# Kernel optimization log

Measured on AMD Instinct MI355X. Metric: run time of the kernel, lower is better.

The kernel has to match this reference:

```python
import jax, jax.numpy as jnp
import numpy as np

EPS = 1e-08
SURROGATE_SCALE = 10.0  # SuperSpike surrogate slope

@jax.custom_vjp
def spike_fn(v):
    # Heaviside forward, SuperSpike surrogate gradient backward
    return (v > 0).astype(v.dtype)

def _spike_fwd(v):
    return spike_fn(v), v

def _spike_bwd(v, g):
    return (g / (1.0 + SURROGATE_SCALE * jnp.abs(v)) ** 2,)

spike_fn.defvjp(_spike_fwd, _spike_bwd)


def setup_inputs() -> dict:
    key = jax.random.key(0)
    k1, k2, k3, k4 = jax.random.split(key, 4)
    B, C, T = 64, 256, 2048
    x = jax.random.normal(k1, (B, C, T), dtype=jnp.float32)
    conv_weight = jax.random.normal(k2, (C, C, 3), dtype=jnp.float32) * 0.05
    beta = jnp.clip(0.7 + 0.01 * jax.random.normal(k3, (1,), dtype=jnp.float32), 0.0, 1.0)
    b = jnp.clip(1.0 + 0.01 * jax.random.normal(k4, (C,), dtype=jnp.float32), 0.0, None)
    return {"x": x, "conv_weight": conv_weight, "beta": beta, "b": b}


def reference(x, conv_weight, beta, b):
    # x: (B, C, T); LIF recurrence over T with scaled threshold/reset
    norm = (conv_weight ** 2).sum((1, 2))          # (C,)
    inv_norm = 1.0 / (norm + EPS)                   # (C,)
    B, C, T = x.shape
    xt = jnp.transpose(x, (2, 0, 1))                # (T, B, C)

    def step(carry, inp):
        mem, spk = carry
        rst = spk * (b * norm)                      # einsum ab,b,b->ab
        mem = (mem - rst) * beta + inp * (1.0 - beta)
        mthr = mem * inv_norm - b
        spk = spike_fn(mthr)
        return (mem, spk), spk

    init = (jnp.zeros((B, C), x.dtype), jnp.zeros((B, C), x.dtype))
    _, spk_rec = jax.lax.scan(step, init, xt)       # (T, B, C)
    return jnp.transpose(spk_rec, (1, 2, 0))        # (B, C, T), flatten_output=False
```

## Files before the change

kernel.cpp:

```cpp
#include <hip/hip_runtime.h>

#define C_DIM 256
#define T_DIM 2048
#define B_DIM 64
#define NROWS (B_DIM * C_DIM)
#define SEGS 8
#define SEGL (T_DIM / SEGS)
#define WARM 128
#define PW   32
#define NPH  ((WARM + SEGL) / PW)
#define WARM_PH (WARM / PW)
#define NSTR 64
#define BUF_F (NSTR * PW)

__device__ __forceinline__ float sqrn(float v) { return __fmul_rn(v, v); }

__global__ __launch_bounds__(64) void norm_kernel(const float* __restrict__ w,
                                                  const float* __restrict__ b,
                                                  float* __restrict__ bn,
                                                  float* __restrict__ ninv) {
    const int c = blockIdx.x;
    const int k = threadIdx.x;
    __shared__ float q[8];
    if (k < 8) {
        const float* a = w + c * 768 + k * 96;
        float r0 = sqrn(a[0]), r1 = sqrn(a[1]), r2 = sqrn(a[2]), r3 = sqrn(a[3]);
        float r4 = sqrn(a[4]), r5 = sqrn(a[5]), r6 = sqrn(a[6]), r7 = sqrn(a[7]);
        #pragma unroll
        for (int i = 8; i < 96; i += 8) {
            r0 = __fadd_rn(r0, sqrn(a[i + 0]));
            r1 = __fadd_rn(r1, sqrn(a[i + 1]));
            r2 = __fadd_rn(r2, sqrn(a[i + 2]));
            r3 = __fadd_rn(r3, sqrn(a[i + 3]));
            r4 = __fadd_rn(r4, sqrn(a[i + 4]));
            r5 = __fadd_rn(r5, sqrn(a[i + 5]));
            r6 = __fadd_rn(r6, sqrn(a[i + 6]));
            r7 = __fadd_rn(r7, sqrn(a[i + 7]));
        }
        q[k] = __fadd_rn(__fadd_rn(__fadd_rn(r0, r1), __fadd_rn(r2, r3)),
                         __fadd_rn(__fadd_rn(r4, r5), __fadd_rn(r6, r7)));
    }
    __syncthreads();
    if (k == 0) {
        float s = __fadd_rn(__fadd_rn(__fadd_rn(q[0], q[1]), __fadd_rn(q[2], q[3])),
                            __fadd_rn(__fadd_rn(q[4], q[5]), __fadd_rn(q[6], q[7])));
        bn[c]   = __fmul_rn(b[c], s);
        ninv[c] = 1.0f / __fadd_rn(s, 1e-8f);
    }
}

__device__ __forceinline__ float step_fast(float xw, float& mem, int& mask,
                                           float bnc, float beta, float nic, float bc) {
    float m0 = __fmul_rn(mem, beta);
    float m1 = __fmul_rn(__fsub_rn(mem, bnc), beta);
    m0 = __fadd_rn(m0, xw);
    m1 = __fadd_rn(m1, xw);
    int mi = (__float_as_int(m1) & mask) | (__float_as_int(m0) & ~mask);
    mem = __int_as_float(mi);
    float p = __fmul_rn(mem, nic);
    float d = __fsub_rn(bc, p);
    mask = __float_as_int(d) >> 31;
    return __int_as_float(mask & 0x3f800000);
}

#define STEP4_NOSTORE(v)                                                   \
    do {                                                                   \
        float xw0 = __fmul_rn((v).x, omb);                                 \
        float xw1 = __fmul_rn((v).y, omb);                                 \
        float xw2 = __fmul_rn((v).z, omb);                                 \
        float xw3 = __fmul_rn((v).w, omb);                                 \
        (void)step_fast(xw0, mem, mask, bnc, beta, nic, bc);               \
        (void)step_fast(xw1, mem, mask, bnc, beta, nic, bc);               \
        (void)step_fast(xw2, mem, mask, bnc, beta, nic, bc);               \
        (void)step_fast(xw3, mem, mask, bnc, beta, nic, bc);               \
    } while (0)

#define STEP4_STORE(v, o)                                                  \
    do {                                                                   \
        float xw0 = __fmul_rn((v).x, omb);                                 \
        float xw1 = __fmul_rn((v).y, omb);                                 \
        float xw2 = __fmul_rn((v).z, omb);                                 \
        float xw3 = __fmul_rn((v).w, omb);                                 \
        (o).x = step_fast(xw0, mem, mask, bnc, beta, nic, bc);             \
        (o).y = step_fast(xw1, mem, mask, bnc, beta, nic, bc);             \
        (o).z = step_fast(xw2, mem, mask, bnc, beta, nic, bc);             \
        (o).w = step_fast(xw3, mem, mask, bnc, beta, nic, bc);             \
    } while (0)

#define WAITCNT_LGKM0  0xC07F
#define WAITVM8()  asm volatile("s_waitcnt vmcnt(8)" ::: "memory")
#define WAITVM16() asm volatile("s_waitcnt vmcnt(16)" ::: "memory")

__device__ __forceinline__ void dma16(const float* gp, float* lp) {
    __builtin_amdgcn_global_load_lds(
        (const __attribute__((address_space(1))) void*)gp,
        (__attribute__((address_space(3))) void*)lp,
        16, 0, 0);
}

__global__ __launch_bounds__(64)
void lif_seg_kernel(const float* __restrict__ x,
                    const float* __restrict__ beta_p,
                    const float* __restrict__ b,
                    const float* __restrict__ bn,
                    const float* __restrict__ ninv,
                    float* __restrict__ out) {
    __shared__ __align__(16) float lds[2 * BUF_F];

    const int lane = threadIdx.x;
    const int seg  = lane & 7;
    const int row  = blockIdx.x * 8 + (lane >> 3);
    const int c    = row & (C_DIM - 1);
    const int lk   = lane & 7;

    const int ds  = lane >> 3;
    const int du  = lane & 7;
    const int swz = du ^ ds;

    const float beta = beta_p[0];
    const float omb  = __fsub_rn(1.0f, beta);
    const float bnc  = bn[c];
    const float nic  = ninv[c];
    const float bc   = b[c];

    float mem = 0.0f;
    int   mask = 0;

    {
        int rel = ds * SEGL - WARM;
        if (rel < 0) rel = 0;
        const float* g = x + rel + 4 * swz;
        #pragma unroll
        for (int q = 0; q < 8; ++q) {
            const size_t grow = (size_t)(blockIdx.x * 8 + q);
            dma16(g + grow * T_DIM, lds + q * (8 * PW));
        }
    }

    #pragma unroll 1
    for (int P = 0; P < NPH; ++P) {
        const int cur = P & 1;
        float* buf = lds + cur * BUF_F;

        if (P + 1 < NPH) {
            int rel = ds * SEGL - WARM + (P + 1) * PW;
            if (rel < 0) rel = 0;
            const float* g = x + rel + 4 * swz;
            float* dst = lds + (cur ^ 1) * BUF_F;
            #pragma unroll
            for (int q = 0; q < 8; ++q) {
                const size_t grow = (size_t)(blockIdx.x * 8 + q);
                dma16(g + grow * T_DIM, dst + q * (8 * PW));
            }
        }

        if (P <= WARM_PH || P == NPH - 1) { WAITVM8(); } else { WAITVM16(); }

        float* my = buf + lane * PW;

        if (P < WARM_PH) {
            #pragma unroll
            for (int g = 0; g < PW / 4; ++g) {
                float4 v = *(const float4*)(my + 4 * (g ^ lk));
                STEP4_NOSTORE(v);
            }
            if (P == WARM_PH - 1) {
                if (seg == 0) { mem = 0.0f; mask = 0; }
            }
        } else {
            #pragma unroll
            for (int g = 0; g < PW / 4; ++g) {
                float4 v = *(const float4*)(my + 4 * (g ^ lk));
                float4 o;
                STEP4_STORE(v, o);
                *(float4*)(my + 4 * (g ^ lk)) = o;
            }
            __builtin_amdgcn_s_waitcnt(WAITCNT_LGKM0);

            const int rel = ds * SEGL - WARM + P * PW;
            #pragma unroll
            for (int q = 0; q < 8; ++q) {
                const size_t grow = (size_t)(blockIdx.x * 8 + q);
                float4 v = *(const float4*)(buf + (8 * q + ds) * PW + 4 * swz);
                *(float4*)(out + grow * T_DIM + rel + 4 * du) = v;
            }
        }
    }
}

extern "C" void kernel_launch(void* const* d_in, const int* in_sizes, int n_in,
                              void* d_out, int out_size, void* d_ws, size_t ws_size,
                              hipStream_t stream) {
    const float* x    = (const float*)d_in[0];
    const float* w    = (const float*)d_in[1];
    const float* beta = (const float*)d_in[2];
    const float* b    = (const float*)d_in[3];
    float* out  = (float*)d_out;
    float* bn   = (float*)d_ws;
    float* ninv = bn + C_DIM;

    norm_kernel<<<C_DIM, 64, 0, stream>>>(w, b, bn, ninv);
    lif_seg_kernel<<<(NROWS * SEGS) / NSTR, NSTR, 0, stream>>>(x, beta, b, bn, ninv, out);
}
```

Baseline: 255.3 us.

## Deepen LDS DMA pipeline to four buffers with smaller phase width

Halves the per-phase time window to 16 steps and switches from double buffering to a 4-deep ring of LDS buffers with three phases of global-to-LDS DMA in flight. The load and store mapping changes to a new XOR swizzle, and the vmcnt waits are retuned per phase. The goal is to hide more global memory latency behind the serial recurrence. In exchange there are twice as many phases, each carrying loop, wait and store overhead, and the outstanding-load accounting is more fragile.

```diff
diff --git a/kernel.cpp b/kernel.cpp
--- a/kernel.cpp
+++ b/kernel.cpp
@@ -7,10 +7,11 @@
 #define SEGS 8
 #define SEGL (T_DIM / SEGS)
 #define WARM 128
-#define PW   32
+#define PW   16
 #define NPH  ((WARM + SEGL) / PW)
 #define WARM_PH (WARM / PW)
 #define NSTR 64
+#define NBUF 4
 #define BUF_F (NSTR * PW)
 
 __device__ __forceinline__ float sqrn(float v) { return __fmul_rn(v, v); }
@@ -88,8 +89,7 @@
     } while (0)
 
 #define WAITCNT_LGKM0  0xC07F
-#define WAITVM8()  asm volatile("s_waitcnt vmcnt(8)" ::: "memory")
-#define WAITVM16() asm volatile("s_waitcnt vmcnt(16)" ::: "memory")
+#define WAITVM(n)  asm volatile("s_waitcnt vmcnt(" #n ")" ::: "memory")
 
 __device__ __forceinline__ void dma16(const float* gp, float* lp) {
     __builtin_amdgcn_global_load_lds(
@@ -105,17 +105,12 @@
                     const float* __restrict__ bn,
                     const float* __restrict__ ninv,
                     float* __restrict__ out) {
-    __shared__ __align__(16) float lds[2 * BUF_F];
+    __shared__ __align__(16) float lds[NBUF * BUF_F];
 
     const int lane = threadIdx.x;
     const int seg  = lane & 7;
-    const int row  = blockIdx.x * 8 + (lane >> 3);
-    const int c    = row & (C_DIM - 1);
-    const int lk   = lane & 7;
-
-    const int ds  = lane >> 3;
-    const int du  = lane & 7;
-    const int swz = du ^ ds;
+    const size_t row = (size_t)blockIdx.x * 8 + (lane >> 3);
+    const int c    = (int)(row & (C_DIM - 1));
 
     const float beta = beta_p[0];
     const float omb  = __fsub_rn(1.0f, beta);
@@ -126,42 +121,54 @@
     float mem = 0.0f;
     int   mask = 0;
 
-    {
-        int rel = ds * SEGL - WARM;
-        if (rel < 0) rel = 0;
-        const float* g = x + rel + 4 * swz;
+
+    #pragma unroll
+    for (int bq = 0; bq < 3; ++bq) {
+        float* dst = lds + bq * BUF_F;
         #pragma unroll
-        for (int q = 0; q < 8; ++q) {
-            const size_t grow = (size_t)(blockIdx.x * 8 + q);
-            dma16(g + grow * T_DIM, lds + q * (8 * PW));
+        for (int j = 0; j < 4; ++j) {
+            const int p  = 64 * j + lane;
+            const int l  = p ^ ((p >> 3) & 7);
+            const int sl = l >> 2, g = l & 3;
+            const size_t srow = (size_t)blockIdx.x * 8 + (sl >> 3);
+            int r = (sl & 7) * SEGL - WARM + bq * PW;
+            if (r < 0) r = 0;
+            dma16(x + srow * T_DIM + r + 4 * g, dst + j * 256);
         }
     }
 
     #pragma unroll 1
     for (int P = 0; P < NPH; ++P) {
-        const int cur = P & 1;
-        float* buf = lds + cur * BUF_F;
-
-        if (P + 1 < NPH) {
-            int rel = ds * SEGL - WARM + (P + 1) * PW;
-            if (rel < 0) rel = 0;
-            const float* g = x + rel + 4 * swz;
-            float* dst = lds + (cur ^ 1) * BUF_F;
-            #pragma unroll
-            for (int q = 0; q < 8; ++q) {
-                const size_t grow = (size_t)(blockIdx.x * 8 + q);
-                dma16(g + grow * T_DIM, dst + q * (8 * PW));
-            }
-        }
-
-        if (P <= WARM_PH || P == NPH - 1) { WAITVM8(); } else { WAITVM16(); }
-
-        float* my = buf + lane * PW;
+        if (P + 3 < NPH) {
+            float* dst = lds + ((P + 3) & 3) * BUF_F;
+            #pragma unroll
+            for (int j = 0; j < 4; ++j) {
+                const int p  = 64 * j + lane;
+                const int l  = p ^ ((p >> 3) & 7);
+                const int sl = l >> 2, g = l & 3;
+                const size_t srow = (size_t)blockIdx.x * 8 + (sl >> 3);
+                int r = (sl & 7) * SEGL - WARM + (P + 3) * PW;
+                if (r < 0) r = 0;
+                dma16(x + srow * T_DIM + r + 4 * g, dst + j * 256);
+            }
+        }
+
+        if      (P <= WARM_PH)     { WAITVM(12); }
+        else if (P == WARM_PH + 1) { WAITVM(16); }
+        else if (P == WARM_PH + 2) { WAITVM(20); }
+        else if (P <= NPH - 4)     { WAITVM(24); }
+        else if (P == NPH - 3)     { WAITVM(20); }
+        else if (P == NPH - 2)     { WAITVM(16); }
+        else                       { WAITVM(12); }
+
+        float* mybuf = lds + (P & 3) * BUF_F;
 
         if (P < WARM_PH) {
             #pragma unroll
-            for (int g = 0; g < PW / 4; ++g) {
-                float4 v = *(const float4*)(my + 4 * (g ^ lk));
+            for (int G = 0; G < PW / 4; ++G) {
+                const int u  = 4 * lane + G;
+                const int ph = u ^ ((u >> 3) & 7);
+                float4 v = *(const float4*)(mybuf + 4 * ph);
                 STEP4_NOSTORE(v);
             }
             if (P == WARM_PH - 1) {
@@ -169,20 +176,26 @@
             }
         } else {
             #pragma unroll
-            for (int g = 0; g < PW / 4; ++g) {
-                float4 v = *(const float4*)(my + 4 * (g ^ lk));
+            for (int G = 0; G < PW / 4; ++G) {
+                const int u  = 4 * lane + G;
+                const int ph = u ^ ((u >> 3) & 7);
+                float* a = mybuf + 4 * ph;
+                float4 v = *(const float4*)a;
                 float4 o;
                 STEP4_STORE(v, o);
-                *(float4*)(my + 4 * (g ^ lk)) = o;
+                *(float4*)a = o;
             }
             __builtin_amdgcn_s_waitcnt(WAITCNT_LGKM0);
 
-            const int rel = ds * SEGL - WARM + P * PW;
-            #pragma unroll
-            for (int q = 0; q < 8; ++q) {
-                const size_t grow = (size_t)(blockIdx.x * 8 + q);
-                float4 v = *(const float4*)(buf + (8 * q + ds) * PW + 4 * swz);
-                *(float4*)(out + grow * T_DIM + rel + 4 * du) = v;
+            #pragma unroll
+            for (int j = 0; j < 4; ++j) {
+                const int p  = 64 * j + lane;
+                const int l  = p ^ ((p >> 3) & 7);
+                const int sl = l >> 2, g = l & 3;
+                const size_t srow = (size_t)blockIdx.x * 8 + (sl >> 3);
+                const int r = (sl & 7) * SEGL - WARM + P * PW;
+                float4 v = *(const float4*)(mybuf + 4 * p);
+                *(float4*)(out + srow * T_DIM + r + 4 * g) = v;
             }
         }
     }
```

Result: slower. 297.8 us (+16.6%).

## Split LIF scan into bit-packed spike kernel and separate float expansion pass

Applied to the files above, without the earlier changes.

The recurrence kernel no longer writes float spikes back through LDS and out to global memory. Instead each stream packs its 32 spikes per phase into one 32-bit word in workspace, and a second kernel expands those words into the float output with coalesced float4 stores. This takes the heavy output store traffic and the LDS round-trip out of the latency-bound scan loop. The cost is an extra kernel launch and a small workspace round-trip. The old path stays as a fallback when the workspace is too small.

```diff
diff --git a/kernel.cpp b/kernel.cpp
--- a/kernel.cpp
+++ b/kernel.cpp
@@ -12,6 +12,8 @@
 #define WARM_PH (WARM / PW)
 #define NSTR 64
 #define BUF_F (NSTR * PW)
+#define NSTREAMS (NROWS * SEGS)
+#define PK_BYTES (NSTREAMS * (SEGL / 32) * 4)
 
 __device__ __forceinline__ float sqrn(float v) { return __fmul_rn(v, v); }
 
@@ -75,6 +77,22 @@
         (void)step_fast(xw3, mem, mask, bnc, beta, nic, bc);               \
     } while (0)
 
+#define STEP4_PACK(v, bp)                                                  \
+    do {                                                                   \
+        float xw0 = __fmul_rn((v).x, omb);                                 \
+        float xw1 = __fmul_rn((v).y, omb);                                 \
+        float xw2 = __fmul_rn((v).z, omb);                                 \
+        float xw3 = __fmul_rn((v).w, omb);                                 \
+        (void)step_fast(xw0, mem, mask, bnc, beta, nic, bc);               \
+        word |= (unsigned)mask & (1u << ((bp) + 0));                       \
+        (void)step_fast(xw1, mem, mask, bnc, beta, nic, bc);               \
+        word |= (unsigned)mask & (1u << ((bp) + 1));                       \
+        (void)step_fast(xw2, mem, mask, bnc, beta, nic, bc);               \
+        word |= (unsigned)mask & (1u << ((bp) + 2));                       \
+        (void)step_fast(xw3, mem, mask, bnc, beta, nic, bc);               \
+        word |= (unsigned)mask & (1u << ((bp) + 3));                       \
+    } while (0)
+
 #define STEP4_STORE(v, o)                                                  \
     do {                                                                   \
         float xw0 = __fmul_rn((v).x, omb);                                 \
@@ -88,14 +106,117 @@
     } while (0)
 
 #define WAITCNT_LGKM0  0xC07F
-#define WAITVM8()  asm volatile("s_waitcnt vmcnt(8)" ::: "memory")
-#define WAITVM16() asm volatile("s_waitcnt vmcnt(16)" ::: "memory")
+#define WAITVM(n)  asm volatile("s_waitcnt vmcnt(" #n ")" ::: "memory")
 
 __device__ __forceinline__ void dma16(const float* gp, float* lp) {
     __builtin_amdgcn_global_load_lds(
         (const __attribute__((address_space(1))) void*)gp,
         (__attribute__((address_space(3))) void*)lp,
         16, 0, 0);
+}
+
+__global__ __launch_bounds__(64)
+void lif_pack_kernel(const float* __restrict__ x,
+                     const float* __restrict__ beta_p,
+                     const float* __restrict__ b,
+                     const float* __restrict__ bn,
+                     const float* __restrict__ ninv,
+                     unsigned* __restrict__ pk) {
+    __shared__ __align__(16) float lds[2 * BUF_F];
+
+    const int lane = threadIdx.x;
+    const int seg  = lane & 7;
+    const size_t row = (size_t)blockIdx.x * 8 + (lane >> 3);
+    const int c    = (int)(row & (C_DIM - 1));
+    const int lk   = lane & 7;
+
+    const int ds  = lane >> 3;
+    const int du  = lane & 7;
+    const int swz = du ^ ds;
+
+    const float beta = beta_p[0];
+    const float omb  = __fsub_rn(1.0f, beta);
+    const float bnc  = bn[c];
+    const float nic  = ninv[c];
+    const float bc   = b[c];
+
+    float mem = 0.0f;
+    int   mask = 0;
+
+    {
+        int rel = ds * SEGL - WARM;
+        if (rel < 0) rel = 0;
+        const float* g = x + rel + 4 * swz;
+        #pragma unroll
+        for (int q = 0; q < 8; ++q) {
+            const size_t grow = (size_t)(blockIdx.x * 8 + q);
+            dma16(g + grow * T_DIM, lds + q * (8 * PW));
+        }
+    }
+
+    #pragma unroll 1
+    for (int P = 0; P < NPH; ++P) {
+        const int cur = P & 1;
+        float* buf = lds + cur * BUF_F;
+
+        if (P + 1 < NPH) {
+            int rel = ds * SEGL - WARM + (P + 1) * PW;
+            if (rel < 0) rel = 0;
+            const float* g = x + rel + 4 * swz;
+            float* dst = lds + (cur ^ 1) * BUF_F;
+            #pragma unroll
+            for (int q = 0; q < 8; ++q) {
+                const size_t grow = (size_t)(blockIdx.x * 8 + q);
+                dma16(g + grow * T_DIM, dst + q * (8 * PW));
+            }
+        }
+
+        if (P + 1 < NPH) { WAITVM(8); } else { WAITVM(0); }
+
+        float* my = buf + lane * PW;
+
+        if (P < WARM_PH) {
+            #pragma unroll
+            for (int g = 0; g < PW / 4; ++g) {
+                float4 v = *(const float4*)(my + 4 * (g ^ lk));
+                STEP4_NOSTORE(v);
+            }
+            if (P == WARM_PH - 1) {
+                if (seg == 0) { mem = 0.0f; mask = 0; }
+            }
+        } else {
+            unsigned word = 0u;
+            #pragma unroll
+            for (int g = 0; g < PW / 4; ++g) {
+                float4 v = *(const float4*)(my + 4 * (g ^ lk));
+                STEP4_PACK(v, 4 * g);
+            }
+            pk[(size_t)(P - WARM_PH) * NSTREAMS + (size_t)blockIdx.x * 64 + lane] = word;
+        }
+    }
+}
+
+__global__ __launch_bounds__(64)
+void expand_kernel(const unsigned* __restrict__ pk, float* __restrict__ out) {
+    const int lane = threadIdx.x;
+    const int shl0 = 31 - 4 * (lane & 7);
+    #pragma unroll 1
+    for (int q = 0; q < 8; ++q) {
+        const size_t row = (size_t)blockIdx.x * 8 + q;
+        const unsigned mine =
+            pk[(size_t)(lane >> 3) * NSTREAMS + row * 8 + (lane & 7)];
+        float* orow = out + row * T_DIM;
+        #pragma unroll
+        for (int i = 0; i < 8; ++i) {
+            const unsigned wv = (unsigned)__shfl((int)mine, (lane & 56) | i, 64);
+            float4 o;
+            o.x = __int_as_float(((int)(wv << (shl0 - 0)) >> 31) & 0x3f800000);
+            o.y = __int_as_float(((int)(wv << (shl0 - 1)) >> 31) & 0x3f800000);
+            o.z = __int_as_float(((int)(wv << (shl0 - 2)) >> 31) & 0x3f800000);
+            o.w = __int_as_float(((int)(wv << (shl0 - 3)) >> 31) & 0x3f800000);
+            *(float4*)(orow + 4 * (64 * i + lane)) = o;
+        }
+    }
 }
 
 __global__ __launch_bounds__(64)
@@ -109,8 +230,8 @@
 
     const int lane = threadIdx.x;
     const int seg  = lane & 7;
-    const int row  = blockIdx.x * 8 + (lane >> 3);
-    const int c    = row & (C_DIM - 1);
+    const size_t row = (size_t)blockIdx.x * 8 + (lane >> 3);
+    const int c    = (int)(row & (C_DIM - 1));
     const int lk   = lane & 7;
 
     const int ds  = lane >> 3;
@@ -154,7 +275,7 @@
             }
         }
 
-        if (P <= WARM_PH || P == NPH - 1) { WAITVM8(); } else { WAITVM16(); }
+        if (P <= WARM_PH || P == NPH - 1) { WAITVM(8); } else { WAITVM(16); }
 
         float* my = buf + lane * PW;
 
@@ -200,5 +321,12 @@
     float* ninv = bn + C_DIM;
 
     norm_kernel<<<C_DIM, 64, 0, stream>>>(w, b, bn, ninv);
-    lif_seg_kernel<<<(NROWS * SEGS) / NSTR, NSTR, 0, stream>>>(x, beta, b, bn, ninv, out);
-}
+
+    if (ws_size >= 4096 + (size_t)PK_BYTES) {
+        unsigned* pk = (unsigned*)((char*)d_ws + 4096);
+        lif_pack_kernel<<<(NROWS * SEGS) / NSTR, NSTR, 0, stream>>>(x, beta, b, bn, ninv, pk);
+        expand_kernel<<<NROWS / 8, NSTR, 0, stream>>>(pk, out);
+    } else {
+        lif_seg_kernel<<<(NROWS * SEGS) / NSTR, NSTR, 0, stream>>>(x, beta, b, bn, ninv, out);
+    }
+}
```

After: 254.6 us. About the same (-0.3%).
